# Kernel optimization log

Measured on AMD Instinct MI355X. Metric: run time of the kernel, lower is better.

The kernel has to match this reference:

```python
import jax, jax.numpy as jnp
import numpy as np
from jax import lax

T = 256            # number of simulated timesteps (= max event timestamp)
DT = 1e-3
TAU_SYN_INV = 200.0
TAU_MEM_INV = 100.0
V_TH = 0.5
ALPHA = 100.0      # SuperSpike surrogate slope

B, S = 32, 8192    # batch, events per sample
IN, H, OUT = 4096, 512, 10
COORD_MAX = 64     # coords in [0,64): event[0]*event[1] < IN


@jax.custom_vjp
def heaviside(x):
    return (x > 0).astype(x.dtype)

def _h_fwd(x):
    return heaviside(x), x

def _h_bwd(x, g):
    # SuperSpike surrogate gradient: 1 / (alpha*|x| + 1)^2
    return (g / (ALPHA * jnp.abs(x) + 1.0) ** 2,)

heaviside.defvjp(_h_fwd, _h_bwd)


def setup_inputs() -> dict:
    key = jax.random.key(0)
    k1, k2, k3, k4, k5, k6, k7 = jax.random.split(key, 7)
    cx = jax.random.randint(k1, (B, S), 0, COORD_MAX)
    cy = jax.random.randint(k2, (B, S), 0, COORD_MAX)
    val = jax.random.randint(k3, (B, S), 0, 2)      # event polarity/value
    ts = jax.random.randint(k4, (B, S), 0, T)       # event timestamp
    x = jnp.stack([cx, cy, val, ts], axis=-1).astype(jnp.int32)  # [B,S,4]
    w_in = jax.random.normal(k5, (H, IN), jnp.float32) * np.float32(np.sqrt(2.0 / IN))
    w_rec = jax.random.normal(k6, (H, H), jnp.float32) * np.float32(np.sqrt(2.0 / H))
    w_out = jax.random.normal(k7, (OUT, H), jnp.float32) * np.float32(np.sqrt(2.0 / H))
    return {"x": x, "w_in": w_in, "w_rec": w_rec, "w_out": w_out}


def reference(x, w_in, w_rec, w_out):
    # --- event -> dense scatter: z[ts, b, x0*x1] = value (later events overwrite) ---
    pos = x[..., 0] * x[..., 1]                      # [B,S] flat input index
    val = x[..., 2].astype(jnp.float32)              # [B,S]
    ts = x[..., 3]                                   # [B,S]
    b_idx = jnp.broadcast_to(jnp.arange(B)[:, None], ts.shape)
    Z = jnp.zeros((T, B, IN), jnp.float32).at[ts, b_idx, pos].set(val)

    leak_i = 1.0 - DT * TAU_SYN_INV

    def step(carry, z_t):
        z_prev, v, i, vo, io = carry
        # LIFRecurrentCell (norse lif_step)
        v_dec = v + DT * TAU_MEM_INV * (-v + i)      # v_leak = 0
        i_dec = i * leak_i
        z_new = heaviside(v_dec - V_TH)
        v_new = (1.0 - z_new) * v_dec                # v_reset = 0
        i_new = i_dec + z_t @ w_in.T + z_prev @ w_rec.T
        # fc_out (no bias)
        y = z_new @ w_out.T
        # LICell (norse li_feed_forward_step): output voltage uses old io
        vo_new = vo + DT * TAU_MEM_INV * (-vo + io)
        io_new = io * leak_i + y
        return (z_new, v_new, i_new, vo_new, io_new), vo_new

    zeros_h = jnp.zeros((B, H), jnp.float32)
    zeros_o = jnp.zeros((B, OUT), jnp.float32)
    init = (zeros_h, zeros_h, zeros_h, zeros_o, zeros_o)
    _, voltages = lax.scan(step, init, Z)            # [T, B, OUT]
    return voltages
```

## Files before the change

kernel.cpp:

```cpp
#include <hip/hip_runtime.h>

#define B_   32
#define S_   8192
#define T_   256
#define IN_  4096
#define H_   512
#define OUT_ 10
#define CAP_ 192
#define Q_   4
#define CH2  16
#define NCH2 (T_ / CH2)
#define PADC (CAP_ + 8)

__global__ void prep_k(const float* __restrict__ w_in, const float* __restrict__ w_rec,
                       const int4* __restrict__ x,
                       float* __restrict__ w_in_T, float* __restrict__ w_rec_T,
                       int* __restrict__ cnt, unsigned* __restrict__ data) {
    int zz = blockIdx.z;
    int tx = threadIdx.x, ty = threadIdx.y;
    if (zz == 2) {
        int flat = blockIdx.y * gridDim.x + blockIdx.x;
        if (flat >= (B_ * S_) / 256) return;
        int e = flat * 256 + ty * 32 + tx;
        int4 ev = x[e];
        int b = e >> 13;
        int s = e & (S_ - 1);
        unsigned pos = (unsigned)(ev.x * ev.y);
        unsigned key = (pos << 14) | ((unsigned)s << 1) | (unsigned)ev.z;
        int bucket = b * T_ + ev.w;
        int slot = atomicAdd(&cnt[bucket], 1);
        if (slot < CAP_) data[bucket * CAP_ + slot] = key;
        return;
    }
    const float* src = zz ? w_rec : w_in;
    float* dst = zz ? w_rec_T : w_in_T;
    const int R = H_, C = zz ? H_ : IN_;
    int bx = blockIdx.x * 32, by = blockIdx.y * 32;
    if (bx >= C || by >= R) return;
    __shared__ float tile[32][33];
    #pragma unroll
    for (int k = 0; k < 32; k += 8) {
        int r = by + ty + k, c = bx + tx;
        if (r < R && c < C) tile[ty + k][tx] = src[(size_t)r * C + c];
    }
    __syncthreads();
    #pragma unroll
    for (int k = 0; k < 32; k += 8) {
        int c = bx + ty + k, r = by + tx;
        if (c < C && r < R) dst[(size_t)c * R + r] = tile[tx][ty + k];
    }
}

__global__ __launch_bounds__(512) void incur_k(const int* __restrict__ cnt,
                                               const unsigned* __restrict__ data,
                                               const float* __restrict__ w_in_T,
                                               float* __restrict__ in_cur) {
    int b  = blockIdx.x / (T_ / Q_);
    int tg = (blockIdx.x % (T_ / Q_)) * Q_;
    __shared__ unsigned keys[Q_][PADC];
    __shared__ unsigned char wf[Q_][PADC];
    __shared__ unsigned short plist[Q_][PADC];
    __shared__ int mq[Q_];
    int tid = threadIdx.x;
    int q = tid >> 7, lt = tid & 127;
    int bucket = b * T_ + tg + q;
    int n = cnt[bucket]; if (n > CAP_) n = CAP_;
    for (int i = lt; i < n; i += 128) keys[q][i] = data[bucket * CAP_ + i];
    #pragma unroll
    for (int i = lt; i < PADC; i += 128) plist[q][i] = (unsigned short)IN_;
    if (lt == 0) mq[q] = 0;
    __syncthreads();
    for (int i = lt; i < n; i += 128) {
        unsigned ki = keys[q][i], pi = ki >> 14;
        bool dead = false;
        for (int j = 0; j < n; j += 4) {
            unsigned a0 = keys[q][j];
            unsigned a1 = keys[q][j + 1 < n ? j + 1 : 0];
            unsigned a2 = keys[q][j + 2 < n ? j + 2 : 0];
            unsigned a3 = keys[q][j + 3 < n ? j + 3 : 0];
            dead |= (((a0 >> 14) == pi) & (a0 > ki));
            dead |= ((j + 1 < n) & ((a1 >> 14) == pi) & (a1 > ki));
            dead |= ((j + 2 < n) & ((a2 >> 14) == pi) & (a2 > ki));
            dead |= ((j + 3 < n) & ((a3 >> 14) == pi) & (a3 > ki));
        }
        wf[q][i] = (unsigned char)(((ki & 1u) != 0u) && !dead);
    }
    __syncthreads();
    for (int i = lt; i < n; i += 128) {
        if (wf[q][i]) {
            unsigned ki = keys[q][i];
            int r = 0;
            for (int j = 0; j < n; j += 4) {
                r += (int)(wf[q][j] && keys[q][j] < ki);
                r += (int)((j + 1 < n) && wf[q][j + 1] && keys[q][j + 1] < ki);
                r += (int)((j + 2 < n) && wf[q][j + 2] && keys[q][j + 2] < ki);
                r += (int)((j + 3 < n) && wf[q][j + 3] && keys[q][j + 3] < ki);
            }
            plist[q][r] = (unsigned short)(ki >> 14);
            atomicAdd(&mq[q], 1);
        }
    }
    __syncthreads();
    int m = mq[q];
    const float4* w4 = (const float4*)w_in_T;
    float4 acc = make_float4(0.f, 0.f, 0.f, 0.f);
    for (int k = 0; k < m; k += 4) {
        float4 g0 = w4[(size_t)plist[q][k + 0] * 128 + lt];
        float4 g1 = w4[(size_t)plist[q][k + 1] * 128 + lt];
        float4 g2 = w4[(size_t)plist[q][k + 2] * 128 + lt];
        float4 g3 = w4[(size_t)plist[q][k + 3] * 128 + lt];
        acc.x = (((acc.x + g0.x) + g1.x) + g2.x) + g3.x;
        acc.y = (((acc.y + g0.y) + g1.y) + g2.y) + g3.y;
        acc.z = (((acc.z + g0.z) + g1.z) + g2.z) + g3.z;
        acc.w = (((acc.w + g0.w) + g1.w) + g2.w) + g3.w;
    }
    ((float4*)(in_cur + (size_t)(tg + q) * (B_ * H_) + b * H_))[lt] = acc;
}

__global__ __launch_bounds__(512) void sim_k(const float* __restrict__ in_cur,
                                             const float* __restrict__ w_rec_T,
                                             const float* __restrict__ w_out,
                                             float* __restrict__ out) {
    int b = blockIdx.x;
    int tid = threadIdx.x, wid = tid >> 6, lane = tid & 63;
    __shared__ unsigned long long mword[2][8];
    const float* icb = in_cur + b * H_ + tid;
    float* outp = out + b * OUT_ + tid;
    float v = 0.f, cur = 0.f, vo = 0.f, io = 0.f;
    bool zst = false;

    float bufA[CH2], bufB[CH2];
    #pragma unroll
    for (int s = 0; s < CH2; ++s) bufA[s] = icb[(size_t)s * (B_ * H_)];
    #pragma unroll
    for (int s = 0; s < CH2; ++s) bufB[s] = icb[(size_t)(CH2 + s) * (B_ * H_)];

#define PROCESS(BUF, CIDX)                                                     \
    do {                                                                       \
        int c_ = (CIDX);                                                       \
        float v0 = v, cur0 = cur, vo0 = vo, io0 = io;                          \
        bool zst0 = zst;                                                       \
        float vmax = -1e30f;                                                   \
        _Pragma("unroll")                                                      \
        for (int s = 0; s < CH2; ++s) {                                        \
            float vd = fmaf(0.1f, cur - v, v);                                 \
            vmax = fmaxf(vmax, vd);                                            \
            v = vd;                                                            \
            cur = cur * 0.8f + BUF[s];                                         \
            if (tid < OUT_) {                                                  \
                float von = fmaf(0.1f, io - vo, vo);                           \
                io *= 0.8f;                                                    \
                outp[(size_t)(c_ * CH2 + s) * (B_ * OUT_)] = von;              \
                vo = von;                                                      \
            }                                                                  \
        }                                                                      \
        int any = __syncthreads_or((vmax > 0.5f) || zst0);                     \
        if (any) {                                                             \
            v = v0; cur = cur0; vo = vo0; io = io0; zst = zst0;                \
            unsigned long long sb = __ballot(zst);                             \
            if (lane == 0) mword[1][wid] = sb;         \
            __syncthreads();                                                   \
            for (int s = 0; s < CH2; ++s) {                                    \
                int p = s & 1;                                                 \
                float vd = fmaf(0.1f, cur - v, v);                             \
                bool z = vd > 0.5f;                                            \
                v = z ? 0.f : vd;                                              \
                unsigned long long bal = __ballot(z);                          \
                if (lane == 0) mword[p][wid] = bal;                            \
                __syncthreads();                                               \
                float c2 = cur * 0.8f + BUF[s];             \
                for (int w = 0; w < 8; ++w) {          \
                    unsigned long long mm = mword[p ^ 1][w];                   \
                    while (mm) {                                               \
                        int j = __builtin_ctzll(mm);                           \
                        c2 += w_rec_T[(size_t)((w << 6) + j) * H_ + tid];      \
                        mm &= mm - 1;                                          \
                    }                                                          \
                }                                                              \
                cur = c2;                                                      \
                if (tid < OUT_) {                                              \
                    float y = 0.f;                                             \
                    for (int w = 0; w < 8; ++w) {         \
                        unsigned long long mm = mword[p][w];                   \
                        while (mm) {                                           \
                            int j = __builtin_ctzll(mm);                       \
                            y += w_out[tid * H_ + (w << 6) + j];               \
                            mm &= mm - 1;                                      \
                        }                                                      \
                    }                                                          \
                    float von = fmaf(0.1f, io - vo, vo);                       \
                    io = io * 0.8f + y;                                        \
                    outp[(size_t)(c_ * CH2 + s) * (B_ * OUT_)] = von;          \
                    vo = von;                                                  \
                }                                                              \
                zst = z;                                                       \
                __syncthreads();                      \
            }                                                                  \
        }                                                                      \
    } while (0)

    for (int c = 0; c < NCH2; c += 2) {
        PROCESS(bufA, c);
        if (c + 2 < NCH2) {
            #pragma unroll
            for (int s = 0; s < CH2; ++s)
                bufA[s] = icb[(size_t)((c + 2) * CH2 + s) * (B_ * H_)];
        }
        PROCESS(bufB, c + 1);
        if (c + 3 < NCH2) {
            #pragma unroll
            for (int s = 0; s < CH2; ++s)
                bufB[s] = icb[(size_t)((c + 3) * CH2 + s) * (B_ * H_)];
        }
    }
#undef PROCESS
}

extern "C" void kernel_launch(void* const* d_in, const int* in_sizes, int n_in,
                              void* d_out, int out_size, void* d_ws, size_t ws_size,
                              hipStream_t stream) {
    const int*   x     = (const int*)d_in[0];
    const float* w_in  = (const float*)d_in[1];
    const float* w_rec = (const float*)d_in[2];
    const float* w_out = (const float*)d_in[3];
    float* out = (float*)d_out;

    char* ws = (char*)d_ws;
    size_t off = 0;
    int*      cnt     = (int*)(ws + off);      off += (size_t)B_ * T_ * 4;
    unsigned* data    = (unsigned*)(ws + off); off += (size_t)B_ * T_ * CAP_ * 4;
    float*    w_in_T  = (float*)(ws + off);    off += (size_t)(IN_ + 1) * H_ * 4;
    float*    w_rec_T = (float*)(ws + off);    off += (size_t)H_ * H_ * 4;
    float*    in_cur  = (float*)(ws + off);    off += (size_t)T_ * B_ * H_ * 4;

    (void)hipMemsetAsync(cnt, 0, (size_t)B_ * T_ * 4, stream);
    (void)hipMemsetAsync(w_in_T + (size_t)IN_ * H_, 0, H_ * 4, stream);

    prep_k<<<dim3(128, 16, 3), dim3(32, 8), 0, stream>>>(w_in, w_rec, (const int4*)x,
                                                         w_in_T, w_rec_T, cnt, data);

    incur_k<<<B_ * (T_ / Q_), 512, 0, stream>>>(cnt, data, w_in_T, in_cur);

    sim_k<<<B_, 512, 0, stream>>>(in_cur, w_rec_T, w_out, out);
}
```

Before: 89.93 us.

## Add no-spike fast path that skips recurrent simulation when no neuron fires

Adds a lightweight parallel kernel that runs the leak dynamics for each hidden neuron across 256 blocks, without recurrence, and records whether any membrane voltage crosses threshold. It zeroes the output for its slice of time steps. The full recurrent simulation then returns early for batch samples that never spike. This removes the serial 32-block recurrent simulation when spikes are absent, which depends on the input statistics, and adds an extra launch plus a pass over in_cur.

```diff
diff --git a/kernel.cpp b/kernel.cpp
--- a/kernel.cpp
+++ b/kernel.cpp
@@ -8,6 +8,7 @@
 #define OUT_ 10
 #define CAP_ 192
 #define Q_   4
+#define FB_  16
 #define CH2  16
 #define NCH2 (T_ / CH2)
 #define PADC (CAP_ + 8)
@@ -117,11 +118,67 @@
     ((float4*)(in_cur + (size_t)(tg + q) * (B_ * H_) + b * H_))[lt] = acc;
 }
 
-__global__ __launch_bounds__(512) void sim_k(const float* __restrict__ in_cur,
-                                             const float* __restrict__ w_rec_T,
-                                             const float* __restrict__ w_out,
-                                             float* __restrict__ out) {
+__global__ __launch_bounds__(64) void simfast_k(const float* __restrict__ in_cur,
+                                                unsigned* __restrict__ flags,
+                                                float* __restrict__ out) {
+    int blk = blockIdx.x;
+    int b = blk >> 3;
+    int slice = blk & 7;
+    int tid = threadIdx.x;
+
+    #pragma unroll
+    for (int i = tid; i < 320; i += 64) {
+        int t = (slice << 5) + i / 10;
+        int o = i - (i / 10) * 10;
+        out[(size_t)t * (B_ * OUT_) + b * OUT_ + o] = 0.f;
+    }
+
+    int h = (slice << 6) + tid;
+    const float* p = in_cur + b * H_ + h;
+    float v = 0.f, cur = 0.f, vmax = -1e30f;
+    float buf0[FB_], buf1[FB_];
+    #pragma unroll
+    for (int s = 0; s < FB_; ++s) buf0[s] = p[(size_t)s * (B_ * H_)];
+    #pragma unroll
+    for (int s = 0; s < FB_; ++s) buf1[s] = p[(size_t)(FB_ + s) * (B_ * H_)];
+
+    for (int t0 = 0; t0 < T_; t0 += 2 * FB_) {
+        #pragma unroll
+        for (int s = 0; s < FB_; ++s) {
+            float vd = fmaf(0.1f, cur - v, v);
+            vmax = fmaxf(vmax, vd);
+            v = vd;
+            cur = cur * 0.8f + buf0[s];
+        }
+        if (t0 + 2 * FB_ < T_) {
+            #pragma unroll
+            for (int s = 0; s < FB_; ++s)
+                buf0[s] = p[(size_t)(t0 + 2 * FB_ + s) * (B_ * H_)];
+        }
+        #pragma unroll
+        for (int s = 0; s < FB_; ++s) {
+            float vd = fmaf(0.1f, cur - v, v);
+            vmax = fmaxf(vmax, vd);
+            v = vd;
+            cur = cur * 0.8f + buf1[s];
+        }
+        if (t0 + 3 * FB_ < T_) {
+            #pragma unroll
+            for (int s = 0; s < FB_; ++s)
+                buf1[s] = p[(size_t)(t0 + 3 * FB_ + s) * (B_ * H_)];
+        }
+    }
+    unsigned long long any = __ballot(vmax > 0.5f);
+    if (tid == 0 && any) atomicOr(&flags[b], 1u);
+}
+
+__global__ __launch_bounds__(512) void simfb_k(const unsigned* __restrict__ flags,
+                                               const float* __restrict__ in_cur,
+                                               const float* __restrict__ w_rec_T,
+                                               const float* __restrict__ w_out,
+                                               float* __restrict__ out) {
     int b = blockIdx.x;
+    if (flags[b] == 0u) return;
     int tid = threadIdx.x, wid = tid >> 6, lane = tid & 63;
     __shared__ unsigned long long mword[2][8];
     const float* icb = in_cur + b * H_ + tid;
@@ -228,12 +285,13 @@
     char* ws = (char*)d_ws;
     size_t off = 0;
     int*      cnt     = (int*)(ws + off);      off += (size_t)B_ * T_ * 4;
+    unsigned* flags   = (unsigned*)(ws + off); off += (size_t)B_ * 4;
     unsigned* data    = (unsigned*)(ws + off); off += (size_t)B_ * T_ * CAP_ * 4;
     float*    w_in_T  = (float*)(ws + off);    off += (size_t)(IN_ + 1) * H_ * 4;
     float*    w_rec_T = (float*)(ws + off);    off += (size_t)H_ * H_ * 4;
     float*    in_cur  = (float*)(ws + off);    off += (size_t)T_ * B_ * H_ * 4;
 
-    (void)hipMemsetAsync(cnt, 0, (size_t)B_ * T_ * 4, stream);
+    (void)hipMemsetAsync(cnt, 0, (size_t)B_ * T_ * 4 + B_ * 4, stream);
     (void)hipMemsetAsync(w_in_T + (size_t)IN_ * H_, 0, H_ * 4, stream);
 
     prep_k<<<dim3(128, 16, 3), dim3(32, 8), 0, stream>>>(w_in, w_rec, (const int4*)x,
@@ -241,5 +299,7 @@
 
     incur_k<<<B_ * (T_ / Q_), 512, 0, stream>>>(cnt, data, w_in_T, in_cur);
 
-    sim_k<<<B_, 512, 0, stream>>>(in_cur, w_rec_T, w_out, out);
-}
+    simfast_k<<<B_ * 8, 64, 0, stream>>>(in_cur, flags, out);
+
+    simfb_k<<<B_, 512, 0, stream>>>(flags, in_cur, w_rec_T, w_out, out);
+}
```

Result: slower. 99.05 us (+10.1%).
